# Kernel optimization log

Hardware: AMD Instinct MI355X
Metric: run time of the kernel (lower is better)

The kernel has to match this reference:

```python
import jax, jax.numpy as jnp
import numpy as np

N_NODES = 100000
N_EDGES = 1600000
K = 5
C = 32
HEADS = 2
LRELU_GAT = 0.2   # SuperGAT negative_slope default
LRELU_OUT = 0.01  # nn.LeakyReLU default
BN_EPS = 1e-5


def setup_inputs() -> dict:
    key = jax.random.key(0)
    ks = jax.random.split(key, 10)
    patch_embs = jax.random.normal(ks[0], (N_NODES, C), dtype=jnp.float32)
    src = jax.random.randint(ks[1], (N_EDGES,), 0, N_NODES, dtype=jnp.int32)
    dst = jax.random.randint(ks[2], (N_EDGES,), 0, N_NODES, dtype=jnp.int32)
    dst = jnp.where(src == dst, (dst + 1) % N_NODES, dst)  # graph has no self-loops
    edge_index = jnp.stack([src, dst])
    edge_attr = jax.random.normal(ks[3], (N_EDGES, 1), dtype=jnp.float32)
    g = 1.0 / np.sqrt(C).astype(np.float32)
    cheb_w = jax.random.normal(ks[4], (K, C, C), dtype=jnp.float32) * g
    cheb_b = jnp.zeros((C,), jnp.float32)
    lin_w = jax.random.normal(ks[5], (C, HEADS * C), dtype=jnp.float32) * g
    att_l = jax.random.normal(ks[6], (HEADS, C), dtype=jnp.float32) * g
    att_r = jax.random.normal(ks[7], (HEADS, C), dtype=jnp.float32) * g
    gat_b = jnp.zeros((C,), jnp.float32)
    bn_g = jnp.ones((C,), jnp.float32)
    bn_b = jnp.zeros((C,), jnp.float32)
    return dict(patch_embs=patch_embs, edge_index=edge_index, edge_attr=edge_attr,
                cheb_w=cheb_w, cheb_b=cheb_b, lin_w=lin_w, att_l=att_l,
                att_r=att_r, gat_b=gat_b, bn_g=bn_g, bn_b=bn_b)


def cheb_conv(x, src, dst, w_edge, cheb_w, cheb_b, n):
    # PyG ChebConv with sym norm, lambda_max=2: L_hat = -D^-1/2 A D^-1/2
    def prop(t):
        return jax.ops.segment_sum(t[src] * w_edge[:, None], dst, num_segments=n)
    Tx0 = x
    out = Tx0 @ cheb_w[0]
    Tx1 = prop(x)
    out = out + Tx1 @ cheb_w[1]
    for k in range(2, cheb_w.shape[0]):
        Tx2 = 2.0 * prop(Tx1) - Tx0
        out = out + Tx2 @ cheb_w[k]
        Tx0, Tx1 = Tx1, Tx2
    return out + cheb_b


def supergat(x, src, dst, lin_w, att_l, att_r, bias, n):
    # SuperGATConv, attention_type='MX', heads=2, concat=False, with self-loops
    H, Ch = att_l.shape
    h = (x @ lin_w).reshape(n, H, Ch)
    xj = h[src]            # [E, H, C] messages from source
    xi = h[dst]            # [E, H, C] target features
    logits = jnp.sum(xi * xj, axis=-1)                         # [E, H]
    alpha = jnp.sum(xj * att_l, -1) + jnp.sum(xi * att_r, -1)  # [E, H]
    alpha = alpha * jax.nn.sigmoid(logits)
    alpha = jax.nn.leaky_relu(alpha, LRELU_GAT)
    # segment softmax over destination nodes
    m = jax.ops.segment_max(alpha, dst, num_segments=n)
    e = jnp.exp(alpha - m[dst])
    s = jax.ops.segment_sum(e, dst, num_segments=n)
    a = e / s[dst]
    out = jax.ops.segment_sum(xj * a[..., None], dst, num_segments=n)  # [N, H, C]
    return out.mean(axis=1) + bias  # concat=False -> head mean


def reference(patch_embs, edge_index, edge_attr, cheb_w, cheb_b, lin_w, att_l,
              att_r, gat_b, bn_g, bn_b):
    n = patch_embs.shape[0]
    src, dst = edge_index[0], edge_index[1]
    # symmetric Laplacian normalization weights
    deg = jax.ops.segment_sum(jnp.ones_like(src, dtype=patch_embs.dtype), src,
                              num_segments=n)
    dis = jnp.where(deg > 0, jax.lax.rsqrt(jnp.maximum(deg, 1.0)), 0.0)
    w_edge = -dis[src] * dis[dst]
    x = cheb_conv(patch_embs, src, dst, w_edge, cheb_w, cheb_b, n)
    # add self-loops for SuperGAT (PyG default add_self_loops=True)
    loop = jnp.arange(n, dtype=src.dtype)
    src2 = jnp.concatenate([src, loop])
    dst2 = jnp.concatenate([dst, loop])
    x2 = supergat(x, src2, dst2, lin_w, att_l, att_r, gat_b, n)
    # LeakyReLU + residual + BatchNorm1d (training-mode batch stats)
    y = jax.nn.leaky_relu(x2, LRELU_OUT) + x2
    mu = y.mean(axis=0)
    var = ((y - mu) ** 2).mean(axis=0)  # biased variance
    return (y - mu) * jax.lax.rsqrt(var + BN_EPS) * bn_g + bn_b
```

## Files before the change

kernel.cpp:

```cpp
#include <hip/hip_runtime.h>
#include <math.h>

#define CC 32
#define CHUNK 4096
#define NCPY 16
#define REDB 1024

static inline int cdiv(long long a, int b) { return (int)((a + b - 1) / b); }

__global__ void k_cnt(const int* __restrict__ src, const int* __restrict__ dst,
                      int* __restrict__ priv, int E, int N) {
  int e = blockIdx.x * blockDim.x + threadIdx.x;
  if (e >= E) return;
  int* p = priv + (size_t)(blockIdx.x & (NCPY - 1)) * N;
  atomicAdd(&p[src[e]], 1 << 16);
  atomicAdd(&p[dst[e]], 1);
}

__global__ void k_reduce(int* __restrict__ priv, float* __restrict__ dis,
                         int* __restrict__ cnt, int* __restrict__ histmat, int N) {
  __shared__ int lh[64];
  if (threadIdx.x < 64) lh[threadIdx.x] = 0;
  __syncthreads();
  int n = blockIdx.x * REDB + threadIdx.x;
  if (n < N) {
    int vals[NCPY];
    int tot = 0;
#pragma unroll
    for (int c = 0; c < NCPY; ++c) {
      vals[c] = priv[(size_t)c * N + n];
      tot += vals[c];
    }
    int deg = tot >> 16, cv = tot & 0xFFFF;
    dis[n] = (deg > 0) ? rsqrtf((float)deg) : 0.f;
    cnt[n] = cv;
    int acc = 0;
#pragma unroll
    for (int c = 0; c < NCPY; ++c) {
      priv[(size_t)c * N + n] = acc;
      acc += vals[c] & 0xFFFF;
    }
    atomicAdd(&lh[min(cv, 63)], 1);
  }
  __syncthreads();
  if (threadIdx.x < 64) histmat[blockIdx.x * 64 + threadIdx.x] = lh[threadIdx.x];
}

__global__ void k_scanhist2(int* __restrict__ histmat, int nb) {
  int lane = threadIdx.x;
  int tot = 0;
  for (int i = 0; i < nb; ++i) tot += histmat[i * 64 + lane];
  __shared__ int sh[64], pf[64];
  sh[lane] = tot;
  __syncthreads();
  if (lane == 0) {
    int acc = 0;
    for (int b = 0; b < 64; ++b) { pf[b] = acc; acc += sh[b]; }
  }
  __syncthreads();
  int acc = pf[lane];
  for (int i = 0; i < nb; ++i) {
    int v = histmat[i * 64 + lane];
    histmat[i * 64 + lane] = acc;
    acc += v;
  }
}

__global__ void k_permfill2(const int* __restrict__ cnt, const int* __restrict__ histmat,
                            int* __restrict__ perm, int N) {
  __shared__ int lh[64], lbase[64];
  if (threadIdx.x < 64) lh[threadIdx.x] = 0;
  __syncthreads();
  int i = blockIdx.x * REDB + threadIdx.x;
  int bin = 0, rank = 0;
  bool act = (i < N);
  if (act) {
    bin = min(cnt[i], 63);
    rank = atomicAdd(&lh[bin], 1);
  }
  __syncthreads();
  if (threadIdx.x < 64) lbase[threadIdx.x] = histmat[blockIdx.x * 64 + threadIdx.x];
  __syncthreads();
  if (act) perm[lbase[bin] + rank] = i;
}

__global__ void k_chunksum(const int* __restrict__ cnt, int* __restrict__ csum, int N) {
  int base = blockIdx.x * CHUNK;
  int v = 0;
  for (int i = threadIdx.x; i < CHUNK; i += 256) {
    int idx = base + i;
    if (idx < N) v += cnt[idx];
  }
  for (int m = 32; m; m >>= 1) v += __shfl_xor(v, m);
  __shared__ int ws[4];
  if ((threadIdx.x & 63) == 0) ws[threadIdx.x >> 6] = v;
  __syncthreads();
  if (threadIdx.x == 0) csum[blockIdx.x] = ws[0] + ws[1] + ws[2] + ws[3];
}

__global__ void k_scancsum(int* __restrict__ csum, int nb, int* __restrict__ rptr,
                           int N, int tot) {
  int acc = 0;
  for (int i = 0; i < nb; ++i) { int v = csum[i]; csum[i] = acc; acc += v; }
  rptr[N] = tot;
}

__global__ void k_fillrptr(int* __restrict__ cnt, const int* __restrict__ csum,
                           int* __restrict__ rptr, int N) {
  int base = blockIdx.x * CHUNK + threadIdx.x * 16;
  int v[16];
  int tot = 0;
#pragma unroll
  for (int q = 0; q < 16; ++q) {
    int idx = base + q;
    v[q] = (idx < N) ? cnt[idx] : 0;
    tot += v[q];
  }
  __shared__ int sh[256];
  sh[threadIdx.x] = tot;
  __syncthreads();
  for (int off = 1; off < 256; off <<= 1) {
    int add = (threadIdx.x >= off) ? sh[threadIdx.x - off] : 0;
    __syncthreads();
    sh[threadIdx.x] += add;
    __syncthreads();
  }
  int excl = sh[threadIdx.x] - tot + csum[blockIdx.x];
#pragma unroll
  for (int q = 0; q < 16; ++q) {
    int idx = base + q;
    if (idx < N) rptr[idx] = excl;
    excl += v[q];
  }
}

__global__ void k_fill3(const int* __restrict__ src, const int* __restrict__ dst,
                        const float* __restrict__ dis, const int* __restrict__ rptr,
                        int* __restrict__ priv, int2* __restrict__ eg, int E, int N) {
  int e = blockIdx.x * blockDim.x + threadIdx.x;
  if (e >= E) return;
  int s = src[e], d = dst[e];
  int* pc = priv + (size_t)(blockIdx.x & (NCPY - 1)) * N;
  int p = rptr[d] + atomicAdd(&pc[d], 1);
  int2 v;
  v.x = s;
  v.y = __float_as_int(-dis[s] * dis[d]);
  eg[p] = v;
}

__global__ void k_cheb4(const float4* __restrict__ x_in4,
                        const float4* __restrict__ x_sub4,
                        const int* __restrict__ rptr, const int2* __restrict__ eg,
                        const float* __restrict__ W, const int* __restrict__ perm,
                        float scale, float4* __restrict__ tx_out4,
                        float4* __restrict__ out4, int N) {
  __shared__ float wl[1024];
  for (int i = threadIdx.x; i < 1024; i += 256) wl[i] = W[i];
  __syncthreads();
  int gid = blockIdx.x * 32 + (threadIdx.x >> 3);
  int lane = threadIdx.x & 7;
  if (gid >= N) return;
  int node = perm[gid];
  int beg = rptr[node], end = rptr[node + 1];
  float tx = 0.f, ty = 0.f, tz = 0.f, tw = 0.f;
  for (int base = beg; base < end; base += 8) {
    int rem = end - base;
    int sj = 0; float wjv = 0.f;
    if (lane < rem) {
      int2 v = eg[base + lane];
      sj = v.x;
      wjv = __int_as_float(v.y);
    }
    if (rem >= 8) {
#pragma unroll
      for (int q = 0; q < 8; ++q) {
        int s = __shfl(sj, q, 8);
        float w = __shfl(wjv, q, 8);
        float4 j4 = x_in4[(long long)s * 8 + lane];
        tx += w * j4.x; ty += w * j4.y; tz += w * j4.z; tw += w * j4.w;
      }
    } else {
      for (int q = 0; q < rem; ++q) {
        int s = __shfl(sj, q, 8);
        float w = __shfl(wjv, q, 8);
        float4 j4 = x_in4[(long long)s * 8 + lane];
        tx += w * j4.x; ty += w * j4.y; tz += w * j4.z; tw += w * j4.w;
      }
    }
  }
  long long o = (long long)node * 8 + lane;
  float ta[4] = {scale * tx, scale * ty, scale * tz, scale * tw};
  if (x_sub4) {
    float4 s4 = x_sub4[o];
    ta[0] -= s4.x; ta[1] -= s4.y; ta[2] -= s4.z; ta[3] -= s4.w;
  }
  if (tx_out4) {
    float4 t4 = {ta[0], ta[1], ta[2], ta[3]};
    tx_out4[o] = t4;
  }
  float4 a4 = out4[o];
  float ax = 0.f, ay = 0.f, az = 0.f, aw = 0.f;
#pragma unroll
  for (int c = 0; c < 32; ++c) {
    float bc = __shfl(ta[c & 3], c >> 2, 8);
    const float4 w4 = *(const float4*)&wl[c * 32 + lane * 4];
    ax += bc * w4.x; ay += bc * w4.y; az += bc * w4.z; aw += bc * w4.w;
  }
  a4.x += ax; a4.y += ay; a4.z += az; a4.w += aw;
  out4[o] = a4;
}

__global__ void k_gemm32b(const float* __restrict__ T, const float* __restrict__ W,
                          const float* __restrict__ bias, float* __restrict__ out,
                          int N) {
  __shared__ float w[1024];
  for (int i = threadIdx.x; i < 1024; i += 256) w[i] = W[i];
  __syncthreads();
  int row = blockIdx.x * 8 + (threadIdx.x >> 5);
  int col = threadIdx.x & 31;
  if (row >= N) return;
  const float* tr = T + (long long)row * 32;
  float acc = 0.f;
#pragma unroll
  for (int c = 0; c < 32; ++c) acc += tr[c] * w[c * 32 + col];
  out[(long long)row * 32 + col] = acc + bias[col];
}

__global__ void k_gemmh(const float* __restrict__ T, const float* __restrict__ W,
                        const float* __restrict__ attl, const float* __restrict__ attr,
                        float* __restrict__ h, float* __restrict__ bl,
                        float* __restrict__ br, int N) {
  __shared__ float w[2048];
  for (int i = threadIdx.x; i < 2048; i += 256) w[i] = W[i];
  __syncthreads();
  int row = blockIdx.x * 4 + (threadIdx.x >> 6);
  int col = threadIdx.x & 63;
  if (row >= N) return;
  const float* tr = T + (long long)row * 32;
  float acc = 0.f;
#pragma unroll
  for (int c = 0; c < 32; ++c) acc += tr[c] * w[c * 64 + col];
  int ch = col & 31, hd = col >> 5;
  h[(long long)row * 64 + (ch & 15) * 4 + (ch >> 4) + 2 * hd] = acc;
  float pl = acc * attl[col], pr = acc * attr[col];
#pragma unroll
  for (int m = 16; m; m >>= 1) {
    pl += __shfl_xor(pl, m, 64);
    pr += __shfl_xor(pr, m, 64);
  }
  if ((col & 31) == 0) {
    bl[row * 2 + (col >> 5)] = pl;
    br[row * 2 + (col >> 5)] = pr;
  }
}

__device__ inline void gat_edge(const float4& j4, const float4& i4, bool hiH,
                                float bxq, float byq, float brh,
                                float& s0, float& s1, float4& v) {
  float d0 = j4.x * i4.x + j4.y * i4.y;
  float d1 = j4.z * i4.z + j4.w * i4.w;
  d0 += __shfl_xor(d0, 8, 16);
  d1 += __shfl_xor(d1, 8, 16);
  float dc = hiH ? d1 : d0;
  dc += __shfl_xor(dc, 4, 16);
  dc += __shfl_xor(dc, 2, 16);
  dc += __shfl_xor(dc, 1, 16);
  float lin = (hiH ? byq : bxq) + brh;
  float a = lin / (1.f + __expf(-dc));
  a = (a > 0.f) ? a : 0.2f * a;
  float ec = __expf(a);
  float e0 = __shfl(ec, 0, 16), e1 = __shfl(ec, 8, 16);
  s0 += e0; s1 += e1;
  v.x += e0 * j4.x; v.y += e0 * j4.y; v.z += e1 * j4.z; v.w += e1 * j4.w;
}

__global__ void k_expgat4(const float4* __restrict__ h4, const int* __restrict__ rptr,
                          const int2* __restrict__ eg, const float2* __restrict__ bl,
                          const float2* __restrict__ br, const float* __restrict__ gb,
                          const int* __restrict__ perm, float* __restrict__ y,
                          float* __restrict__ bns, int N) {
  __shared__ float ls[64];
  for (int i = threadIdx.x; i < 64; i += 256) ls[i] = 0.f;
  __syncthreads();
  int gid = blockIdx.x * 16 + (threadIdx.x >> 4);
  int lane = threadIdx.x & 15;
  if (gid < N) {
    int node = perm[gid];
    float4 i4 = h4[(long long)node * 16 + lane];
    float2 brn = br[node], bln = bl[node];
    bool hiH = (lane & 8) != 0;
    float brh = hiH ? brn.y : brn.x;
    float s0 = 0.f, s1 = 0.f;
    float4 v = {0.f, 0.f, 0.f, 0.f};
    gat_edge(i4, i4, hiH, bln.x, bln.y, brh, s0, s1, v);
    int beg = rptr[node], end = rptr[node + 1];
    for (int base = beg; base < end; base += 16) {
      int rem = end - base;
      int sj = 0; float bx = 0.f, by = 0.f;
      if (lane < rem) {
        sj = eg[base + lane].x;
        float2 b2 = bl[sj];
        bx = b2.x; by = b2.y;
      }
      if (rem >= 16) {
#pragma unroll
        for (int p = 0; p < 8; ++p) {
          int qA = p * 2, qB = p * 2 + 1;
          int sA = __shfl(sj, qA, 16);
          int sB = __shfl(sj, qB, 16);
          float4 jA = h4[(long long)sA * 16 + lane];
          float4 jB = h4[(long long)sB * 16 + lane];
          float bxA = __shfl(bx, qA, 16), byA = __shfl(by, qA, 16);
          float bxB = __shfl(bx, qB, 16), byB = __shfl(by, qB, 16);
          gat_edge(jA, i4, hiH, bxA, byA, brh, s0, s1, v);
          gat_edge(jB, i4, hiH, bxB, byB, brh, s0, s1, v);
        }
      } else {
        int q = 0;
        for (; q + 2 <= rem; q += 2) {
          int sA = __shfl(sj, q, 16);
          int sB = __shfl(sj, q + 1, 16);
          float4 jA = h4[(long long)sA * 16 + lane];
          float4 jB = h4[(long long)sB * 16 + lane];
          float bxA = __shfl(bx, q, 16), byA = __shfl(by, q, 16);
          float bxB = __shfl(bx, q + 1, 16), byB = __shfl(by, q + 1, 16);
          gat_edge(jA, i4, hiH, bxA, byA, brh, s0, s1, v);
          gat_edge(jB, i4, hiH, bxB, byB, brh, s0, s1, v);
        }
        if (q < rem) {
          int sA = __shfl(sj, q, 16);
          float4 jA = h4[(long long)sA * 16 + lane];
          float bxA = __shfl(bx, q, 16), byA = __shfl(by, q, 16);
          gat_edge(jA, i4, hiH, bxA, byA, brh, s0, s1, v);
        }
      }
    }
    float x2a = 0.5f * (v.x / s0 + v.z / s1) + gb[lane];
    float x2b = 0.5f * (v.y / s0 + v.w / s1) + gb[lane + 16];
    float ya = ((x2a > 0.f) ? x2a : 0.01f * x2a) + x2a;
    float yb = ((x2b > 0.f) ? x2b : 0.01f * x2b) + x2b;
    y[(long long)node * 32 + lane] = ya;
    y[(long long)node * 32 + lane + 16] = yb;
    atomicAdd(&ls[lane], ya);
    atomicAdd(&ls[lane + 16], yb);
    atomicAdd(&ls[32 + lane], ya * ya);
    atomicAdd(&ls[32 + lane + 16], yb * yb);
  }
  __syncthreads();
  if (threadIdx.x < 64) atomicAdd(&bns[threadIdx.x], ls[threadIdx.x]);
}

__global__ void k_bnfinal(const float* __restrict__ y, const float* __restrict__ bns,
                          const float* __restrict__ g, const float* __restrict__ b,
                          float* __restrict__ out, int N) {
  int i = blockIdx.x * blockDim.x + threadIdx.x;
  if (i >= N * CC) return;
  int c = i & 31;
  float inv_n = 1.f / (float)N;
  float mu = bns[c] * inv_n;
  float var = bns[32 + c] * inv_n - mu * mu;
  out[i] = (y[i] - mu) * rsqrtf(var + 1e-5f) * g[c] + b[c];
}

extern "C" void kernel_launch(void* const* d_in, const int* in_sizes, int n_in,
                              void* d_out, int out_size, void* d_ws, size_t ws_size,
                              hipStream_t stream) {
  const float* patch = (const float*)d_in[0];
  const int* eidx = (const int*)d_in[1];
  const float* cheb_w = (const float*)d_in[3];
  const float* cheb_b = (const float*)d_in[4];
  const float* lin_w = (const float*)d_in[5];
  const float* att_l = (const float*)d_in[6];
  const float* att_r = (const float*)d_in[7];
  const float* gat_b = (const float*)d_in[8];
  const float* bn_g = (const float*)d_in[9];
  const float* bn_b = (const float*)d_in[10];
  float* out = (float*)d_out;

  const int N = in_sizes[0] / CC;
  const int E = in_sizes[1] / 2;
  const int* src = eidx;
  const int* dst = eidx + E;

  float* R0 = (float*)d_ws;
  float* R1 = R0 + (size_t)N * 32;
  int2* eg = (int2*)(R1 + (size_t)N * 32);
  int* grptr = (int*)(eg + E);
  int* cnt = grptr + (N + 2);
  int* csum = cnt + N;
  float* dis = (float*)(csum + 64);
  float* bns = dis + N;
  int* perm = (int*)(bns + 64);
  float* bl = (float*)(perm + N);
  float* br = bl + (size_t)N * 2;
  int* priv = (int*)(br + (size_t)N * 2);
  int* histmat = priv + (size_t)NCPY * N;
  float* h = R0;

  const int B = 256;
  const long long NC = (long long)N * 32;
  int nbred = cdiv(N, REDB);

  hipMemsetAsync(priv, 0, sizeof(int) * (size_t)NCPY * N, stream);
  hipMemsetAsync(bns, 0, sizeof(float) * 64, stream);

  k_cnt<<<cdiv(E, B), B, 0, stream>>>(src, dst, priv, E, N);
  k_reduce<<<nbred, REDB, 0, stream>>>(priv, dis, cnt, histmat, N);
  k_scanhist2<<<1, 64, 0, stream>>>(histmat, nbred);
  k_permfill2<<<nbred, REDB, 0, stream>>>(cnt, histmat, perm, N);

  int nb = cdiv(N, CHUNK);
  k_chunksum<<<nb, B, 0, stream>>>(cnt, csum, N);
  k_scancsum<<<1, 1, 0, stream>>>(csum, nb, grptr, N, E);
  k_fillrptr<<<nb, B, 0, stream>>>(cnt, csum, grptr, N);
  k_fill3<<<cdiv(E, B), B, 0, stream>>>(src, dst, dis, grptr, priv, eg, E, N);

  k_gemm32b<<<cdiv(N, 8), B, 0, stream>>>(patch, cheb_w, cheb_b, out, N);
  k_cheb4<<<cdiv(N, 32), B, 0, stream>>>((const float4*)patch, nullptr, grptr, eg,
                                         cheb_w + 1024, perm, 1.f,
                                         (float4*)R0, (float4*)out, N);
  k_cheb4<<<cdiv(N, 32), B, 0, stream>>>((const float4*)R0, (const float4*)patch,
                                         grptr, eg, cheb_w + 2048, perm, 2.f,
                                         (float4*)R1, (float4*)out, N);
  k_cheb4<<<cdiv(N, 32), B, 0, stream>>>((const float4*)R1, (const float4*)R0,
                                         grptr, eg, cheb_w + 3072, perm, 2.f,
                                         (float4*)R0, (float4*)out, N);
  k_cheb4<<<cdiv(N, 32), B, 0, stream>>>((const float4*)R0, (const float4*)R1,
                                         grptr, eg, cheb_w + 4096, perm, 2.f,
                                         nullptr, (float4*)out, N);

  k_gemmh<<<cdiv(N, 4), B, 0, stream>>>(out, lin_w, att_l, att_r, h, bl, br, N);
  k_expgat4<<<cdiv(N, 16), B, 0, stream>>>((const float4*)h, grptr, eg,
                                           (const float2*)bl, (const float2*)br,
                                           gat_b, perm, out, bns, N);
  k_bnfinal<<<cdiv(NC, B), B, 0, stream>>>(out, bns, bn_g, bn_b, out, N);
}
```

Before: 699.6 us.

## Store GAT features in fp16, unroll edge loop by four, reverse node order

```diff
diff --git a/kernel.cpp b/kernel.cpp
--- a/kernel.cpp
+++ b/kernel.cpp
@@ -1,4 +1,5 @@
 #include <hip/hip_runtime.h>
+#include <hip/hip_fp16.h>
 #include <math.h>
 
 #define CC 32
@@ -160,7 +161,7 @@
   int gid = blockIdx.x * 32 + (threadIdx.x >> 3);
   int lane = threadIdx.x & 7;
   if (gid >= N) return;
-  int node = perm[gid];
+  int node = perm[N - 1 - gid];
   int beg = rptr[node], end = rptr[node + 1];
   float tx = 0.f, ty = 0.f, tz = 0.f, tw = 0.f;
   for (int base = beg; base < end; base += 8) {
@@ -228,7 +229,7 @@
 
 __global__ void k_gemmh(const float* __restrict__ T, const float* __restrict__ W,
                         const float* __restrict__ attl, const float* __restrict__ attr,
-                        float* __restrict__ h, float* __restrict__ bl,
+                        __half* __restrict__ h, float* __restrict__ bl,
                         float* __restrict__ br, int N) {
   __shared__ float w[2048];
   for (int i = threadIdx.x; i < 2048; i += 256) w[i] = W[i];
@@ -241,7 +242,7 @@
 #pragma unroll
   for (int c = 0; c < 32; ++c) acc += tr[c] * w[c * 64 + col];
   int ch = col & 31, hd = col >> 5;
-  h[(long long)row * 64 + (ch & 15) * 4 + (ch >> 4) + 2 * hd] = acc;
+  h[(long long)row * 64 + (ch & 15) * 4 + (ch >> 4) + 2 * hd] = __float2half(acc);
   float pl = acc * attl[col], pr = acc * attr[col];
 #pragma unroll
   for (int m = 16; m; m >>= 1) {
@@ -252,6 +253,13 @@
     bl[row * 2 + (col >> 5)] = pl;
     br[row * 2 + (col >> 5)] = pr;
   }
+}
+
+__device__ inline float4 h4f(int2 r) {
+  __half2 lo = *reinterpret_cast<__half2*>(&r.x);
+  __half2 hi = *reinterpret_cast<__half2*>(&r.y);
+  float2 a = __half22float2(lo), b = __half22float2(hi);
+  return make_float4(a.x, a.y, b.x, b.y);
 }
 
 __device__ inline void gat_edge(const float4& j4, const float4& i4, bool hiH,
@@ -274,7 +282,7 @@
   v.x += e0 * j4.x; v.y += e0 * j4.y; v.z += e1 * j4.z; v.w += e1 * j4.w;
 }
 
-__global__ void k_expgat4(const float4* __restrict__ h4, const int* __restrict__ rptr,
+__global__ void k_expgat4(const int2* __restrict__ h2, const int* __restrict__ rptr,
                           const int2* __restrict__ eg, const float2* __restrict__ bl,
                           const float2* __restrict__ br, const float* __restrict__ gb,
                           const int* __restrict__ perm, float* __restrict__ y,
@@ -285,8 +293,8 @@
   int gid = blockIdx.x * 16 + (threadIdx.x >> 4);
   int lane = threadIdx.x & 15;
   if (gid < N) {
-    int node = perm[gid];
-    float4 i4 = h4[(long long)node * 16 + lane];
+    int node = perm[N - 1 - gid];
+    float4 i4 = h4f(h2[(long long)node * 16 + lane]);
     float2 brn = br[node], bln = bl[node];
     bool hiH = (lane & 8) != 0;
     float brh = hiH ? brn.y : brn.x;
@@ -304,34 +312,42 @@
       }
       if (rem >= 16) {
 #pragma unroll
-        for (int p = 0; p < 8; ++p) {
-          int qA = p * 2, qB = p * 2 + 1;
-          int sA = __shfl(sj, qA, 16);
-          int sB = __shfl(sj, qB, 16);
-          float4 jA = h4[(long long)sA * 16 + lane];
-          float4 jB = h4[(long long)sB * 16 + lane];
-          float bxA = __shfl(bx, qA, 16), byA = __shfl(by, qA, 16);
-          float bxB = __shfl(bx, qB, 16), byB = __shfl(by, qB, 16);
-          gat_edge(jA, i4, hiH, bxA, byA, brh, s0, s1, v);
-          gat_edge(jB, i4, hiH, bxB, byB, brh, s0, s1, v);
+        for (int p = 0; p < 4; ++p) {
+          int q0 = p * 4, q1 = q0 + 1, q2 = q0 + 2, q3 = q0 + 3;
+          int sA = __shfl(sj, q0, 16);
+          int sB = __shfl(sj, q1, 16);
+          int sC = __shfl(sj, q2, 16);
+          int sD = __shfl(sj, q3, 16);
+          int2 rA = h2[(long long)sA * 16 + lane];
+          int2 rB = h2[(long long)sB * 16 + lane];
+          int2 rC = h2[(long long)sC * 16 + lane];
+          int2 rD = h2[(long long)sD * 16 + lane];
+          float bxA = __shfl(bx, q0, 16), byA = __shfl(by, q0, 16);
+          float bxB = __shfl(bx, q1, 16), byB = __shfl(by, q1, 16);
+          float bxC = __shfl(bx, q2, 16), byC = __shfl(by, q2, 16);
+          float bxD = __shfl(bx, q3, 16), byD = __shfl(by, q3, 16);
+          gat_edge(h4f(rA), i4, hiH, bxA, byA, brh, s0, s1, v);
+          gat_edge(h4f(rB), i4, hiH, bxB, byB, brh, s0, s1, v);
+          gat_edge(h4f(rC), i4, hiH, bxC, byC, brh, s0, s1, v);
+          gat_edge(h4f(rD), i4, hiH, bxD, byD, brh, s0, s1, v);
         }
       } else {
         int q = 0;
         for (; q + 2 <= rem; q += 2) {
           int sA = __shfl(sj, q, 16);
           int sB = __shfl(sj, q + 1, 16);
-          float4 jA = h4[(long long)sA * 16 + lane];
-          float4 jB = h4[(long long)sB * 16 + lane];
+          int2 rA = h2[(long long)sA * 16 + lane];
+          int2 rB = h2[(long long)sB * 16 + lane];
           float bxA = __shfl(bx, q, 16), byA = __shfl(by, q, 16);
           float bxB = __shfl(bx, q + 1, 16), byB = __shfl(by, q + 1, 16);
-          gat_edge(jA, i4, hiH, bxA, byA, brh, s0, s1, v);
-          gat_edge(jB, i4, hiH, bxB, byB, brh, s0, s1, v);
+          gat_edge(h4f(rA), i4, hiH, bxA, byA, brh, s0, s1, v);
+          gat_edge(h4f(rB), i4, hiH, bxB, byB, brh, s0, s1, v);
         }
         if (q < rem) {
           int sA = __shfl(sj, q, 16);
-          float4 jA = h4[(long long)sA * 16 + lane];
+          int2 rA = h2[(long long)sA * 16 + lane];
           float bxA = __shfl(bx, q, 16), byA = __shfl(by, q, 16);
-          gat_edge(jA, i4, hiH, bxA, byA, brh, s0, s1, v);
+          gat_edge(h4f(rA), i4, hiH, bxA, byA, brh, s0, s1, v);
         }
       }
     }
@@ -395,7 +411,7 @@
   float* br = bl + (size_t)N * 2;
   int* priv = (int*)(br + (size_t)N * 2);
   int* histmat = priv + (size_t)NCPY * N;
-  float* h = R0;
+  __half* h = (__half*)R0;
 
   const int B = 256;
   const long long NC = (long long)N * 32;
@@ -430,7 +446,7 @@
                                          nullptr, (float4*)out, N);
 
   k_gemmh<<<cdiv(N, 4), B, 0, stream>>>(out, lin_w, att_l, att_r, h, bl, br, N);
-  k_expgat4<<<cdiv(N, 16), B, 0, stream>>>((const float4*)h, grptr, eg,
+  k_expgat4<<<cdiv(N, 16), B, 0, stream>>>((const int2*)h, grptr, eg,
                                            (const float2*)bl, (const float2*)br,
                                            gat_b, perm, out, bns, N);
   k_bnfinal<<<cdiv(NC, B), B, 0, stream>>>(out, bns, bn_g, bn_b, out, N);
```

After: 701.5 us. No clear change (+0.3%).
